# Kernel optimization log

Measured on AMD Instinct MI355X. Metric: run time of the kernel, lower is better.

## Reference

```python
import jax, jax.numpy as jnp
import numpy as np

EMB = 1024
HEADS = 16
HEAD_DIM = EMB // HEADS


def setup_inputs() -> dict:
    key = jax.random.key(0)
    ks = jax.random.split(key, 9)
    s = 1.0 / np.sqrt(EMB)  # torch Linear default init scale (uniform), use normal*s for simplicity of magnitude
    x = jax.random.normal(ks[0], (2, 2048, EMB), dtype=jnp.float32)
    wQ = jax.random.uniform(ks[1], (EMB, EMB), jnp.float32, -s, s)
    bQ = jax.random.uniform(ks[2], (EMB,), jnp.float32, -s, s)
    wK = jax.random.uniform(ks[3], (EMB, EMB), jnp.float32, -s, s)
    bK = jax.random.uniform(ks[4], (EMB,), jnp.float32, -s, s)
    wV = jax.random.uniform(ks[5], (EMB, EMB), jnp.float32, -s, s)
    bV = jax.random.uniform(ks[6], (EMB,), jnp.float32, -s, s)
    wO = jax.random.uniform(ks[7], (EMB, EMB), jnp.float32, -s, s)
    bO = jax.random.uniform(ks[8], (EMB,), jnp.float32, -s, s)
    return {"x": x, "wQ": wQ, "bQ": bQ, "wK": wK, "bK": bK, "wV": wV, "bV": bV, "wO": wO, "bO": bO}


def reference(x, wQ, bQ, wK, bK, wV, bV, wO, bO):
    B, S, E = x.shape
    H, Dh = HEADS, HEAD_DIM
    # manual LayerNorm-like scaling; torch.std uses unbiased (ddof=1)
    mu = jnp.mean(x, axis=-1, keepdims=True)
    sd = jnp.std(x, axis=-1, keepdims=True, ddof=1)
    xn = (x - mu) / (sd + 1e-6)
    # torch Linear: y = x @ W.T + b
    q = (xn @ wQ.T + bQ).reshape(B, S, H, Dh).transpose(0, 2, 1, 3)  # [B,H,S,Dh]
    k = (xn @ wK.T + bK).reshape(B, S, H, Dh).transpose(0, 2, 1, 3)
    v = (xn @ wV.T + bV).reshape(B, S, H, Dh).transpose(0, 2, 1, 3)
    scores = jnp.einsum('bhsd,bhtd->bhst', q, k) / np.sqrt(Dh).astype(np.float32)
    A = jax.nn.softmax(scores, axis=-1)
    Hout = jnp.einsum('bhst,bhtd->bhsd', A, v)  # [B,H,S,Dh]
    Hout = Hout.transpose(0, 2, 1, 3).reshape(B, S, E)
    return Hout @ wO.T + bO
```

## Files before the change

kernel.cpp:

```cpp
#include <hip/hip_runtime.h>
#include <cstdint>
#include <cstddef>

typedef __bf16 bf16x8 __attribute__((ext_vector_type(8)));
typedef float f32x4 __attribute__((ext_vector_type(4)));
typedef unsigned short us4 __attribute__((ext_vector_type(4)));
typedef unsigned short us8 __attribute__((ext_vector_type(8)));
typedef unsigned int ui4 __attribute__((ext_vector_type(4)));
typedef unsigned short u16;

#define QSCALE 0.18033688011112042f

#define MFMA16(a, b, c) __builtin_amdgcn_mfma_f32_16x16x32_bf16((a), (b), (c), 0, 0, 0)
#define GLOAD16(g, l)                                                        \
  __builtin_amdgcn_global_load_lds(                                          \
      (const __attribute__((address_space(1))) void*)(g),                    \
      (__attribute__((address_space(3))) void*)(l), 16, 0, 0)

__device__ __forceinline__ u16 f2bf(float x) {
  unsigned int u = __float_as_uint(x);
  unsigned int r = u + 0x7fffu + ((u >> 16) & 1u);
  return (u16)(r >> 16);
}

__global__ __launch_bounds__(256) void prep_kernel(
    const float* __restrict__ x, const float* __restrict__ wq,
    const float* __restrict__ wk, const float* __restrict__ wv,
    const float* __restrict__ wo, u16* __restrict__ xn,
    u16* __restrict__ wdst) {
  const int bid = blockIdx.x;
  const int t = threadIdx.x;
  if (bid < 4096) {
    const int row = bid;
    const float* xr = x + (size_t)row * 1024;
    float4 v = *(const float4*)(xr + t * 4);
    float s = v.x + v.y + v.z + v.w;
    float s2 = v.x * v.x + v.y * v.y + v.z * v.z + v.w * v.w;
#pragma unroll
    for (int o = 32; o >= 1; o >>= 1) {
      s += __shfl_xor(s, o);
      s2 += __shfl_xor(s2, o);
    }
    __shared__ float red[8];
    const int wv_ = t >> 6, ln = t & 63;
    if (ln == 0) {
      red[wv_] = s;
      red[4 + wv_] = s2;
    }
    __syncthreads();
    s = red[0] + red[1] + red[2] + red[3];
    s2 = red[4] + red[5] + red[6] + red[7];
    const float mu = s * (1.0f / 1024.0f);
    float var = (s2 - 1024.0f * mu * mu) * (1.0f / 1023.0f);
    var = fmaxf(var, 0.0f);
    const float inv = 1.0f / (sqrtf(var) + 1e-6f);
    us4 o;
    o.x = f2bf((v.x - mu) * inv);
    o.y = f2bf((v.y - mu) * inv);
    o.z = f2bf((v.z - mu) * inv);
    o.w = f2bf((v.w - mu) * inv);
    *(us4*)(xn + (size_t)row * 1024 + t * 4) = o;
  } else {
    const int wid = bid - 4096;
    const int mat = wid >> 9, xi = wid & 511;
    const float* src = (mat == 0) ? wq : (mat == 1) ? wk : (mat == 2) ? wv : wo;
    const float sc = (mat == 0) ? QSCALE : 1.0f;
    u16* d = wdst + ((size_t)mat << 20);
    const size_t i = ((size_t)xi * 256 + t) * 8;
    float4 a = *(const float4*)(src + i);
    float4 b = *(const float4*)(src + i + 4);
    us8 o;
    o[0] = f2bf(a.x * sc);
    o[1] = f2bf(a.y * sc);
    o[2] = f2bf(a.z * sc);
    o[3] = f2bf(a.w * sc);
    o[4] = f2bf(b.x * sc);
    o[5] = f2bf(b.y * sc);
    o[6] = f2bf(b.z * sc);
    o[7] = f2bf(b.w * sc);
    *(us8*)(d + i) = o;
  }
}

__device__ __forceinline__ void gemm_sbuf_core(const u16* __restrict__ A,
                                               const u16* __restrict__ W,
                                               int m0, int n0,
                                               u16* __restrict__ As,
                                               u16* __restrict__ Bs,
                                               f32x4 acc[2][4]) {
  const int tid = threadIdx.x;
  const int lane = tid & 63, wave = tid >> 6;
  const int wm = wave >> 1, wn = wave & 1;
  const int lr = lane & 15, lg = lane >> 4;

  for (int kt = 0; kt < 16; ++kt) {
#pragma unroll
    for (int i = 0; i < 2; i++) {
      const int idx = i * 256 + tid;
      const int r = idx >> 3, c = idx & 7;
      GLOAD16(A + (size_t)(m0 + r) * 1024 + kt * 64 + (c ^ (r & 7)) * 8,
              &As[idx * 8]);
    }
#pragma unroll
    for (int i = 0; i < 4; i++) {
      const int idx = i * 256 + tid;
      const int r = idx >> 3, c = idx & 7;
      GLOAD16(W + (size_t)(n0 + r) * 1024 + kt * 64 + (c ^ (r & 7)) * 8,
              &Bs[idx * 8]);
    }
    __syncthreads();
#pragma unroll
    for (int ks = 0; ks < 2; ks++) {
      const int co = ((ks * 4 + lg) ^ (lr & 7)) * 8;
      bf16x8 af[2], bfr[4];
#pragma unroll
      for (int m = 0; m < 2; m++)
        af[m] = *(const bf16x8*)&As[(wm * 32 + m * 16 + lr) * 64 + co];
#pragma unroll
      for (int n = 0; n < 4; n++)
        bfr[n] = *(const bf16x8*)&Bs[(wn * 64 + n * 16 + lr) * 64 + co];
#pragma unroll
      for (int m = 0; m < 2; m++)
#pragma unroll
        for (int n = 0; n < 4; n++)
          acc[m][n] = MFMA16(af[m], bfr[n], acc[m][n]);
    }
    __syncthreads();
  }
}

__global__ __launch_bounds__(256, 6) void qkv_gemm(
    const u16* __restrict__ xn, const u16* __restrict__ Wall,
    const float* __restrict__ bQ, const float* __restrict__ bK,
    const float* __restrict__ bV, u16* __restrict__ Qb, u16* __restrict__ Kb,
    u16* __restrict__ VTb) {
  __shared__ u16 As[64 * 64];
  __shared__ u16 Bs[128 * 64];
  const int z = blockIdx.z;
  const u16* W = Wall + ((size_t)z << 20);
  const float* bias = (z == 0) ? bQ : (z == 1) ? bK : bV;
  const float bscale = (z == 0) ? QSCALE : 1.0f;
  const int m0 = blockIdx.x * 64, n0 = blockIdx.y * 128;
  f32x4 acc[2][4] = {};
  gemm_sbuf_core(xn, W, m0, n0, As, Bs, acc);

  const int lane = threadIdx.x & 63, wave = threadIdx.x >> 6;
  const int wm = wave >> 1, wn = wave & 1, lr = lane & 15, lg = lane >> 4;
  if (z == 2) {
#pragma unroll
    for (int n = 0; n < 4; n++) {
      const int col = n0 + wn * 64 + n * 16 + lr;
      const float bv = bias[col];
      const int hh = col >> 6, d = col & 63;
#pragma unroll
      for (int m = 0; m < 2; m++) {
        const int rb = m0 + wm * 32 + m * 16 + lg * 4;
#pragma unroll
        for (int j = 0; j < 4; j++) {
          const int row = rb + j;
          const int bb = row >> 11, s = row & 2047;
          VTb[(((size_t)(bb * 16 + hh) * 64 + d) << 11) + s] =
              f2bf(acc[m][n][j] + bv);
        }
      }
    }
  } else {
    u16* o = (z == 0) ? Qb : Kb;
#pragma unroll
    for (int n = 0; n < 4; n++) {
      const int col = n0 + wn * 64 + n * 16 + lr;
      const float bv = bias[col] * bscale;
#pragma unroll
      for (int m = 0; m < 2; m++) {
        const int rb = m0 + wm * 32 + m * 16 + lg * 4;
#pragma unroll
        for (int j = 0; j < 4; j++)
          o[(size_t)(rb + j) * 1024 + col] = f2bf(acc[m][n][j] + bv);
      }
    }
  }
}

__device__ __forceinline__ void gemm64_core(const u16* __restrict__ A,
                                            const u16* __restrict__ W,
                                            int m0, int n0,
                                            u16 (*As)[64 * 32],
                                            u16 (*Bs)[128 * 32],
                                            f32x4 acc[2][4]) {
  const int tid = threadIdx.x;
  const int lane = tid & 63, wave = tid >> 6;
  const int wm = wave >> 1, wn = wave & 1;
  const int lr = lane & 15, lg = lane >> 4;

  auto stage = [&](int buf, int kt) {
    {
      const int row = tid >> 2, ch = tid & 3;
      const int sc = ch ^ ((row >> 1) & 3);
      GLOAD16(A + (size_t)(m0 + row) * 1024 + kt * 32 + sc * 8,
              &As[buf][tid * 8]);
    }
#pragma unroll
    for (int i = 0; i < 2; i++) {
      const int idx = i * 256 + tid;
      const int row = idx >> 2, ch = idx & 3;
      const int sc = ch ^ ((row >> 1) & 3);
      GLOAD16(W + (size_t)(n0 + row) * 1024 + kt * 32 + sc * 8,
              &Bs[buf][idx * 8]);
    }
  };

  stage(0, 0);
  const int cs = (lg ^ ((lr >> 1) & 3)) * 8;
  int cur = 0;
  for (int kt = 0; kt < 32; ++kt) {
    __syncthreads();
    if (kt + 1 < 32) stage(cur ^ 1, kt + 1);
    bf16x8 af[2], bfr[4];
#pragma unroll
    for (int m = 0; m < 2; m++)
      af[m] = *(const bf16x8*)&As[cur][(wm * 32 + m * 16 + lr) * 32 + cs];
#pragma unroll
    for (int n = 0; n < 4; n++)
      bfr[n] = *(const bf16x8*)&Bs[cur][(wn * 64 + n * 16 + lr) * 32 + cs];
#pragma unroll
    for (int m = 0; m < 2; m++)
#pragma unroll
      for (int n = 0; n < 4; n++)
        acc[m][n] = MFMA16(af[m], bfr[n], acc[m][n]);
    cur ^= 1;
  }
}

__global__ __launch_bounds__(256, 5) void o_gemm(const u16* __restrict__ A,
                                                 const u16* __restrict__ W,
                                                 const float* __restrict__ bias,
                                                 float* __restrict__ out) {
  __shared__ u16 As[2][64 * 32];
  __shared__ u16 Bs[2][128 * 32];
  const int m0 = blockIdx.x * 64, n0 = blockIdx.y * 128;
  f32x4 acc[2][4] = {};
  gemm64_core(A, W, m0, n0, As, Bs, acc);
  const int lane = threadIdx.x & 63, wave = threadIdx.x >> 6;
  const int wm = wave >> 1, wn = wave & 1, lr = lane & 15, lg = lane >> 4;
#pragma unroll
  for (int n = 0; n < 4; n++) {
    const int col = n0 + wn * 64 + n * 16 + lr;
    const float bv = bias[col];
#pragma unroll
    for (int m = 0; m < 2; m++) {
      const int rb = m0 + wm * 32 + m * 16 + lg * 4;
#pragma unroll
      for (int j = 0; j < 4; j++)
        out[(size_t)(rb + j) * 1024 + col] = acc[m][n][j] + bv;
    }
  }
}

__global__ __launch_bounds__(256, 2) void attn_kernel(
    const u16* __restrict__ Qb, const u16* __restrict__ Kb,
    const u16* __restrict__ VTb, u16* __restrict__ Hb) {
  __shared__ u16 Ks[2][128 * 64];
  __shared__ u16 Vs[2][64 * 128];
  const int tid = threadIdx.x;
  const int wave = tid >> 6, lane = tid & 63;
  const int lr = lane & 15, lg = lane >> 4;
  const int qb = blockIdx.x, bh = blockIdx.y;
  const int b = bh >> 4, h = bh & 15;

  bf16x8 aq[2][2];
#pragma unroll
  for (int qg = 0; qg < 2; qg++) {
    const int qrow = b * 2048 + qb * 128 + wave * 32 + qg * 16 + lr;
    const u16* qsrc = Qb + (size_t)qrow * 1024 + h * 64 + lg * 8;
    aq[qg][0] = *(const bf16x8*)qsrc;
    aq[qg][1] = *(const bf16x8*)(qsrc + 32);
  }

  f32x4 oacc[2][4] = {};
  f32x4 lacc[2] = {};
  const ui4 ones_u = {0x3f803f80u, 0x3f803f80u, 0x3f803f80u, 0x3f803f80u};
  const bf16x8 ones = __builtin_bit_cast(bf16x8, ones_u);

  auto stage = [&](int buf, int kt) {
#pragma unroll
    for (int i = 0; i < 4; i++) {
      const int idx = i * 256 + tid;
      const int r = idx >> 3, c = idx & 7;
      GLOAD16(Kb + (size_t)(b * 2048 + kt * 128 + r) * 1024 + h * 64 +
                  (c ^ (r & 7)) * 8,
              &Ks[buf][idx * 8]);
    }
#pragma unroll
    for (int i = 0; i < 4; i++) {
      const int idx = i * 256 + tid;
      const int r = idx >> 4, c = idx & 15;
      GLOAD16(VTb + (size_t)(bh * 64 + r) * 2048 + kt * 128 +
                  (c ^ (r & 7)) * 8,
              &Vs[buf][idx * 8]);
    }
  };

  auto softpack = [&](f32x4 (&s)[8], ui4 (&pf)[4]) {
#pragma unroll
    for (int n = 0; n < 8; n++)
#pragma unroll
      for (int j = 0; j < 4; j++)
        s[n][j] = __builtin_amdgcn_exp2f(s[n][j]);
    unsigned int w[8][2];
#pragma unroll
    for (int n = 0; n < 8; n++) {
      asm("v_cvt_pk_bf16_f32 %0, %1, %2"
          : "=v"(w[n][0])
          : "v"(s[n][0]), "v"(s[n][1]));
      asm("v_cvt_pk_bf16_f32 %0, %1, %2"
          : "=v"(w[n][1])
          : "v"(s[n][2]), "v"(s[n][3]));
    }
#pragma unroll
    for (int ks = 0; ks < 4; ks++) {
      unsigned int pw[4];
#pragma unroll
      for (int rp = 0; rp < 2; rp++) {
        unsigned int a = w[2 * ks][rp], bb = w[2 * ks + 1][rp];
        asm("v_permlane32_swap_b32 %0, %1" : "+v"(a), "+v"(bb));
        asm("v_permlane16_swap_b32 %0, %1" : "+v"(a), "+v"(bb));
        pw[rp] = a;
        pw[2 + rp] = bb;
      }
      pf[ks] = (ui4){pw[0], pw[1], pw[2], pw[3]};
    }
  };

  stage(0, 0);
  int cur = 0;
  for (int kt = 0; kt < 16; ++kt) {
    __syncthreads();
    if (kt + 1 < 16) stage(cur ^ 1, kt + 1);

    f32x4 s0[8], s1[8];
#pragma unroll
    for (int n = 0; n < 8; n++) {
      s0[n] = (f32x4){0.f, 0.f, 0.f, 0.f};
      s1[n] = (f32x4){0.f, 0.f, 0.f, 0.f};
    }
    __builtin_amdgcn_s_setprio(1);
#pragma unroll
    for (int n = 0; n < 8; n++) {
      const int row = n * 16 + lr;
#pragma unroll
      for (int ks = 0; ks < 2; ks++) {
        const int byo = (ks * 64 + lg * 16) ^ ((row & 7) << 4);
        const bf16x8 kfr = *(const bf16x8*)&Ks[cur][row * 64 + (byo >> 1)];
        s0[n] = MFMA16(kfr, aq[0][ks], s0[n]);
        s1[n] = MFMA16(kfr, aq[1][ks], s1[n]);
      }
    }
    __builtin_amdgcn_s_setprio(0);

    ui4 pf0[4], pf1[4];
    softpack(s0, pf0);
    softpack(s1, pf1);

    __builtin_amdgcn_s_setprio(1);
#pragma unroll
    for (int ks = 0; ks < 4; ks++) {
      const bf16x8 p0 = __builtin_bit_cast(bf16x8, pf0[ks]);
      const bf16x8 p1 = __builtin_bit_cast(bf16x8, pf1[ks]);
#pragma unroll
      for (int n = 0; n < 4; n++) {
        const int row = n * 16 + lr;
        const int byo = (ks * 64 + lg * 16) ^ ((row & 7) << 4);
        const bf16x8 vb = *(const bf16x8*)&Vs[cur][row * 128 + (byo >> 1)];
        oacc[0][n] = MFMA16(p0, vb, oacc[0][n]);
        oacc[1][n] = MFMA16(p1, vb, oacc[1][n]);
      }
      lacc[0] = MFMA16(p0, ones, lacc[0]);
      lacc[1] = MFMA16(p1, ones, lacc[1]);
    }
    __builtin_amdgcn_s_setprio(0);
    cur ^= 1;
  }

#pragma unroll
  for (int qg = 0; qg < 2; qg++) {
    float rl[4];
#pragma unroll
    for (int j = 0; j < 4; j++) rl[j] = 1.0f / lacc[qg][j];
    const int hrow_base = b * 2048 + qb * 128 + wave * 32 + qg * 16 + lg * 4;
#pragma unroll
    for (int n = 0; n < 4; n++) {
      const int col = h * 64 + n * 16 + lr;
#pragma unroll
      for (int j = 0; j < 4; j++) {
        const float val = oacc[qg][n][j] * rl[j];
        Hb[(size_t)(hrow_base + j) * 1024 + col] = f2bf(val);
      }
    }
  }
}

extern "C" void kernel_launch(void* const* d_in, const int* in_sizes, int n_in,
                              void* d_out, int out_size, void* d_ws,
                              size_t ws_size, hipStream_t stream) {
  const float* x = (const float*)d_in[0];
  const float* wQ = (const float*)d_in[1];
  const float* bQ = (const float*)d_in[2];
  const float* wK = (const float*)d_in[3];
  const float* bK = (const float*)d_in[4];
  const float* wV = (const float*)d_in[5];
  const float* bV = (const float*)d_in[6];
  const float* wO = (const float*)d_in[7];
  const float* bO = (const float*)d_in[8];
  float* out = (float*)d_out;

  char* ws = (char*)d_ws;
  u16* xn = (u16*)(ws);
  u16* Wall = (u16*)(ws + ((size_t)8 << 20));
  u16* Qb = (u16*)(ws + ((size_t)16 << 20));
  u16* Kb = (u16*)(ws + ((size_t)24 << 20));
  u16* VTb = (u16*)(ws + ((size_t)32 << 20));
  u16* Hb = (u16*)(ws + ((size_t)40 << 20));

  prep_kernel<<<6144, 256, 0, stream>>>(x, wQ, wK, wV, wO, xn, Wall);
  qkv_gemm<<<dim3(64, 8, 3), 256, 0, stream>>>(xn, Wall, bQ, bK, bV, Qb, Kb,
                                               VTb);
  attn_kernel<<<dim3(16, 32), 256, 0, stream>>>(Qb, Kb, VTb, Hb);
  o_gemm<<<dim3(64, 8), 256, 0, stream>>>(Hb, Wall + ((size_t)3 << 20), bO,
                                          out);
}
```

Measured before the change: 128.8 us.

## Double-buffer QKV GEMM LDS tiles and split attention V tile into halves

The QKV projection GEMM now double-buffers its A and B LDS tiles, issuing the next k-tile's async global-to-LDS loads right after the barrier and dropping the trailing barrier. This is meant to overlap global memory latency with MFMA work, at the cost of twice the shared memory per block, so the launch-bounds occupancy hint drops from 6 to 3. Separately, the attention kernel's V^T tile is stored as two 64-wide halves with a 64-element row stride and matching swizzle, changing the LDS layout and bank pattern for V reads.

```diff
diff --git a/kernel.cpp b/kernel.cpp
--- a/kernel.cpp
+++ b/kernel.cpp
@@ -82,67 +82,73 @@
   }
 }
 
-__device__ __forceinline__ void gemm_sbuf_core(const u16* __restrict__ A,
+__device__ __forceinline__ void gemm64k64_core(const u16* __restrict__ A,
                                                const u16* __restrict__ W,
                                                int m0, int n0,
-                                               u16* __restrict__ As,
-                                               u16* __restrict__ Bs,
+                                               u16 (*As)[64 * 64],
+                                               u16 (*Bs)[128 * 64],
                                                f32x4 acc[2][4]) {
   const int tid = threadIdx.x;
   const int lane = tid & 63, wave = tid >> 6;
   const int wm = wave >> 1, wn = wave & 1;
   const int lr = lane & 15, lg = lane >> 4;
 
-  for (int kt = 0; kt < 16; ++kt) {
+  auto stage = [&](int buf, int kt) {
 #pragma unroll
     for (int i = 0; i < 2; i++) {
       const int idx = i * 256 + tid;
       const int r = idx >> 3, c = idx & 7;
       GLOAD16(A + (size_t)(m0 + r) * 1024 + kt * 64 + (c ^ (r & 7)) * 8,
-              &As[idx * 8]);
+              &As[buf][idx * 8]);
     }
 #pragma unroll
     for (int i = 0; i < 4; i++) {
       const int idx = i * 256 + tid;
       const int r = idx >> 3, c = idx & 7;
       GLOAD16(W + (size_t)(n0 + r) * 1024 + kt * 64 + (c ^ (r & 7)) * 8,
-              &Bs[idx * 8]);
-    }
+              &Bs[buf][idx * 8]);
+    }
+  };
+
+  stage(0, 0);
+  int cur = 0;
+  for (int kt = 0; kt < 16; ++kt) {
     __syncthreads();
+    if (kt + 1 < 16) stage(cur ^ 1, kt + 1);
 #pragma unroll
     for (int ks = 0; ks < 2; ks++) {
       const int co = ((ks * 4 + lg) ^ (lr & 7)) * 8;
       bf16x8 af[2], bfr[4];
 #pragma unroll
       for (int m = 0; m < 2; m++)
-        af[m] = *(const bf16x8*)&As[(wm * 32 + m * 16 + lr) * 64 + co];
+        af[m] = *(const bf16x8*)&As[cur][(wm * 32 + m * 16 + lr) * 64 + co];
 #pragma unroll
       for (int n = 0; n < 4; n++)
-        bfr[n] = *(const bf16x8*)&Bs[(wn * 64 + n * 16 + lr) * 64 + co];
+        bfr[n] = *(const bf16x8*)&Bs[cur][(wn * 64 + n * 16 + lr) * 64 + co];
 #pragma unroll
       for (int m = 0; m < 2; m++)
 #pragma unroll
         for (int n = 0; n < 4; n++)
           acc[m][n] = MFMA16(af[m], bfr[n], acc[m][n]);
     }
-    __syncthreads();
-  }
-}
-
-__global__ __launch_bounds__(256, 6) void qkv_gemm(
+    cur ^= 1;
+  }
+}
+
+__global__ __launch_bounds__(256, 3) void qkv_gemm(
     const u16* __restrict__ xn, const u16* __restrict__ Wall,
     const float* __restrict__ bQ, const float* __restrict__ bK,
     const float* __restrict__ bV, u16* __restrict__ Qb, u16* __restrict__ Kb,
     u16* __restrict__ VTb) {
-  __shared__ u16 As[64 * 64];
-  __shared__ u16 Bs[128 * 64];
+  __shared__ u16 As[2][64 * 64];
+  __shared__ u16 Bs[2][128 * 64];
   const int z = blockIdx.z;
   const u16* W = Wall + ((size_t)z << 20);
   const float* bias = (z == 0) ? bQ : (z == 1) ? bK : bV;
   const float bscale = (z == 0) ? QSCALE : 1.0f;
   const int m0 = blockIdx.x * 64, n0 = blockIdx.y * 128;
   f32x4 acc[2][4] = {};
-  gemm_sbuf_core(xn, W, m0, n0, As, Bs, acc);
+  gemm64k64_core(xn, W, m0, n0, As, Bs, acc);
 
   const int lane = threadIdx.x & 63, wave = threadIdx.x >> 6;
   const int wm = wave >> 1, wn = wave & 1, lr = lane & 15, lg = lane >> 4;
@@ -260,7 +266,7 @@
     const u16* __restrict__ Qb, const u16* __restrict__ Kb,
     const u16* __restrict__ VTb, u16* __restrict__ Hb) {
   __shared__ u16 Ks[2][128 * 64];
-  __shared__ u16 Vs[2][64 * 128];
+  __shared__ u16 Vs[2][2][64 * 64];
   const int tid = threadIdx.x;
   const int wave = tid >> 6, lane = tid & 63;
   const int lr = lane & 15, lg = lane >> 4;
@@ -291,12 +297,15 @@
               &Ks[buf][idx * 8]);
     }
 #pragma unroll
-    for (int i = 0; i < 4; i++) {
-      const int idx = i * 256 + tid;
-      const int r = idx >> 4, c = idx & 15;
-      GLOAD16(VTb + (size_t)(bh * 64 + r) * 2048 + kt * 128 +
-                  (c ^ (r & 7)) * 8,
-              &Vs[buf][idx * 8]);
+    for (int half = 0; half < 2; half++) {
+#pragma unroll
+      for (int i = 0; i < 2; i++) {
+        const int jdx = i * 256 + tid;
+        const int r = jdx >> 3, lc = jdx & 7;
+        GLOAD16(VTb + (size_t)(bh * 64 + r) * 2048 + kt * 128 +
+                    (half * 8 + (lc ^ (r & 7))) * 8,
+                &Vs[buf][half][jdx * 8]);
+      }
     }
   };
 
@@ -364,13 +373,14 @@
     __builtin_amdgcn_s_setprio(1);
 #pragma unroll
     for (int ks = 0; ks < 4; ks++) {
+      const int half = ks >> 1, ks2 = ks & 1;
       const bf16x8 p0 = __builtin_bit_cast(bf16x8, pf0[ks]);
       const bf16x8 p1 = __builtin_bit_cast(bf16x8, pf1[ks]);
 #pragma unroll
       for (int n = 0; n < 4; n++) {
         const int row = n * 16 + lr;
-        const int byo = (ks * 64 + lg * 16) ^ ((row & 7) << 4);
-        const bf16x8 vb = *(const bf16x8*)&Vs[cur][row * 128 + (byo >> 1)];
+        const int ch = ((ks2 * 4 + lg) ^ (row & 7)) * 8;
+        const bf16x8 vb = *(const bf16x8*)&Vs[cur][half][row * 64 + ch];
         oacc[0][n] = MFMA16(p0, vb, oacc[0][n]);
         oacc[1][n] = MFMA16(p1, vb, oacc[1][n]);
       }
```

New measurement: 113.1 us. -12.1%, faster.
